# Kernel optimization log

Hardware: AMD Instinct MI355X
Metric: run time of the kernel (lower is better)

## Reference

```python
import jax, jax.numpy as jnp
import numpy as np

NUM_HEADS = 2

def mha(q, k, v, w_in, b_in, w_out, b_out):
    # torch nn.MultiheadAttention with batch_first=True, packed in_proj
    E = q.shape[-1]
    Dh = E // NUM_HEADS
    wq, wk, wv = jnp.split(w_in, 3, axis=0)
    bq, bk, bv = jnp.split(b_in, 3, axis=0)
    qh = (q @ wq.T + bq).reshape(q.shape[0], q.shape[1], NUM_HEADS, Dh)
    kh = (k @ wk.T + bk).reshape(k.shape[0], k.shape[1], NUM_HEADS, Dh)
    vh = (v @ wv.T + bv).reshape(v.shape[0], v.shape[1], NUM_HEADS, Dh)
    scores = jnp.einsum('blhd,bmhd->bhlm', qh, kh) / jnp.sqrt(jnp.asarray(Dh, q.dtype))
    attn = jax.nn.softmax(scores, axis=-1)
    ctx = jnp.einsum('bhlm,bmhd->blhd', attn, vh).reshape(q.shape[0], q.shape[1], E)
    return ctx @ w_out.T + b_out


def setup_inputs() -> dict:
    key = jax.random.key(0)
    ks = jax.random.split(key, 10)
    B, S, F, E, H = 16384, 512, 4, 8, 16
    s = 0.3
    return {
        'x': jax.random.normal(ks[0], (B, S, E), jnp.float32),
        'Q': jax.random.normal(ks[1], (F, E), jnp.float32) * s,
        'sa_w_in': jax.random.normal(ks[2], (3 * E, E), jnp.float32) * s,
        'sa_b_in': jnp.zeros((3 * E,), jnp.float32),
        'sa_w_out': jax.random.normal(ks[3], (E, E), jnp.float32) * s,
        'sa_b_out': jnp.zeros((E,), jnp.float32),
        'ca_w_in': jax.random.normal(ks[4], (3 * E, E), jnp.float32) * s,
        'ca_b_in': jnp.zeros((3 * E,), jnp.float32),
        'ca_w_out': jax.random.normal(ks[5], (E, E), jnp.float32) * s,
        'ca_b_out': jnp.zeros((E,), jnp.float32),
        'r_w1': jax.random.normal(ks[6], (H, F * E), jnp.float32) * s,
        'r_b1': jnp.zeros((H,), jnp.float32),
        'r_w2': jax.random.normal(ks[7], (1, H), jnp.float32) * s,
        'r_b2': jnp.zeros((1,), jnp.float32),
    }


def reference(x, Q, sa_w_in, sa_b_in, sa_w_out, sa_b_out,
              ca_w_in, ca_b_in, ca_w_out, ca_b_out,
              r_w1, r_b1, r_w2, r_b2):
    B = x.shape[0]
    # self-attention over the (batch-identical) factor queries
    Qb = jnp.broadcast_to(Q[None], (B,) + Q.shape)  # [B, F, E]
    Q_upd = mha(Qb, Qb, Qb, sa_w_in, sa_b_in, sa_w_out, sa_b_out)
    # cross-attention: factors attend over the input sequence
    Q_cross = mha(Q_upd, x, x, ca_w_in, ca_b_in, ca_w_out, ca_b_out)  # [B, F, E]
    similarity = jnp.einsum('bfe,bse->bfs', Q_cross, x)  # [B, F, S]
    attn_weights = jax.nn.softmax(similarity, axis=-1)
    final_factors = jnp.einsum('bfs,bse->bfe', attn_weights, x)  # [B, F, E]
    fused = final_factors.reshape(B, -1)  # [B, F*E]
    h = jax.nn.relu(fused @ r_w1.T + r_b1)
    out = h @ r_w2.T + r_b2  # [B, 1]
    return out, similarity
```

## Files before the change

kernel.cpp:

```cpp
#include <hip/hip_runtime.h>

#define SEQ 512
#define EMB 8
#define NFAC 4


__global__ void precompute_kernel(
    const float* __restrict__ Q,
    const float* __restrict__ sa_w_in, const float* __restrict__ sa_b_in,
    const float* __restrict__ sa_w_out, const float* __restrict__ sa_b_out,
    const float* __restrict__ ca_w_in, const float* __restrict__ ca_b_in,
    const float* __restrict__ ca_w_out, const float* __restrict__ ca_b_out,
    float* __restrict__ ws)
{
    const int t = threadIdx.x;
    __shared__ float sw[608];
    __shared__ float sqh[32], skh[32], svh[32], sctx[32], sQu[32], sqc[32];
    enum { OQ = 0, SWIN = 32, SBIN = 224, SWOUT = 248, SBOUT = 312,
           CWIN = 320, CBIN = 512, CWOUT = 536, CBOUT = 600 };

    for (int i = t; i < 32;  i += 64) sw[OQ + i]    = Q[i];
    for (int i = t; i < 192; i += 64) sw[SWIN + i]  = sa_w_in[i];
    for (int i = t; i < 24;  i += 64) sw[SBIN + i]  = sa_b_in[i];
    for (int i = t; i < 64;  i += 64) sw[SWOUT + i] = sa_w_out[i];
    if (t < 8) sw[SBOUT + t] = sa_b_out[t];
    for (int i = t; i < 192; i += 64) sw[CWIN + i]  = ca_w_in[i];
    for (int i = t; i < 24;  i += 64) sw[CBIN + i]  = ca_b_in[i];
    for (int i = t; i < 64;  i += 64) sw[CWOUT + i] = ca_w_out[i];
    if (t < 8) sw[CBOUT + t] = ca_b_out[t];
    __syncthreads();

    {
        const int e2 = t >> 3, e = t & 7;
        float m0 = 0.f, m1 = 0.f;
        #pragma unroll
        for (int d = 0; d < 4; ++d) {
            m0 += sw[CWOUT + e2 * 8 + d]     * sw[CWIN + (16 + d) * 8 + e];
            m1 += sw[CWOUT + e2 * 8 + 4 + d] * sw[CWIN + (20 + d) * 8 + e];
        }
        ws[72 + t]  = m0;
        ws[136 + t] = m1;
    }
    if (t < 8) {
        float a = sw[CBOUT + t];
        #pragma unroll
        for (int d = 0; d < 8; ++d) a += sw[CWOUT + t * 8 + d] * sw[CBIN + 16 + d];
        ws[200 + t] = a;
    }

    if (t < 32) {
        const int l = t >> 3, j = t & 7;
        float aq = sw[SBIN + j], ak = sw[SBIN + 8 + j], av = sw[SBIN + 16 + j];
        #pragma unroll
        for (int e = 0; e < 8; ++e) {
            const float q = sw[OQ + l * 8 + e];
            aq += q * sw[SWIN + j * 8 + e];
            ak += q * sw[SWIN + (8 + j) * 8 + e];
            av += q * sw[SWIN + (16 + j) * 8 + e];
        }
        sqh[t] = aq; skh[t] = ak; svh[t] = av;
    }
    __syncthreads();

    if (t < 8) {
        const int h = t >> 2, l = t & 3;
        float sc[4], mx = -1e30f;
        #pragma unroll
        for (int m = 0; m < 4; ++m) {
            float a = 0.f;
            #pragma unroll
            for (int d = 0; d < 4; ++d) a += sqh[l * 8 + h * 4 + d] * skh[m * 8 + h * 4 + d];
            sc[m] = 0.5f * a;
            mx = fmaxf(mx, sc[m]);
        }
        float ssum = 0.f;
        #pragma unroll
        for (int m = 0; m < 4; ++m) { sc[m] = __expf(sc[m] - mx); ssum += sc[m]; }
        const float inv = 1.f / ssum;
        #pragma unroll
        for (int d = 0; d < 4; ++d) {
            float a = 0.f;
            #pragma unroll
            for (int m = 0; m < 4; ++m) a += sc[m] * svh[m * 8 + h * 4 + d];
            sctx[l * 8 + h * 4 + d] = a * inv;
        }
    }
    __syncthreads();

    if (t < 32) {
        const int l = t >> 3, e2 = t & 7;
        float a = sw[SBOUT + e2];
        #pragma unroll
        for (int e = 0; e < 8; ++e) a += sctx[l * 8 + e] * sw[SWOUT + e2 * 8 + e];
        sQu[l * 8 + e2] = a;
    }
    __syncthreads();

    if (t < 32) {
        const int l = t >> 3, j = t & 7;
        float a = sw[CBIN + j];
        #pragma unroll
        for (int e = 0; e < 8; ++e) a += sQu[l * 8 + e] * sw[CWIN + j * 8 + e];
        sqc[l * 8 + j] = a;
    }
    __syncthreads();

    {
        const int p = t >> 3, e = t & 7, h = p >> 2, f = p & 3;
        float a = 0.f;
        #pragma unroll
        for (int d = 0; d < 4; ++d)
            a += sqc[f * 8 + h * 4 + d] * sw[CWIN + (8 + h * 4 + d) * 8 + e];
        ws[p * 8 + e] = 0.5f * a;
    }
    if (t < 8) {
        const int p = t, h = p >> 2, f = p & 3;
        float a = 0.f;
        #pragma unroll
        for (int d = 0; d < 4; ++d) a += sqc[f * 8 + h * 4 + d] * sw[CBIN + 8 + h * 4 + d];
        ws[64 + p] = 0.5f * a;
    }
}

__global__ __launch_bounds__(256, 4) void fused_kernel(
    const float* __restrict__ x,
    const float* __restrict__ r_w1, const float* __restrict__ r_b1,
    const float* __restrict__ r_w2, const float* __restrict__ r_b2,
    const float* __restrict__ ws,
    float* __restrict__ out, float* __restrict__ sim_out)
{
    const int b = blockIdx.x;
    const int tid = threadIdx.x;
    const int w = __builtin_amdgcn_readfirstlane(tid >> 6);
    const int lane = tid & 63;

    __shared__ float4 su4[16];
    __shared__ float sff[4][8];

    const float* xb = x + (size_t)b * (SEQ * EMB);

    const int p0 = 2 * w, p1 = 2 * w + 1;
    float wq0[8], wq1[8];
    #pragma unroll
    for (int e = 0; e < 8; ++e) { wq0[e] = ws[p0 * 8 + e]; wq1[e] = ws[p1 * 8 + e]; }
    const float cb0 = ws[64 + p0], cb1 = ws[64 + p1];

    float xr[8][8];
    float xa0[8] = {0.f,0.f,0.f,0.f,0.f,0.f,0.f,0.f};
    float xa1[8] = {0.f,0.f,0.f,0.f,0.f,0.f,0.f,0.f};
    float sum0 = 0.f, sum1 = 0.f;
    #pragma unroll
    for (int j = 0; j < 8; ++j) {
        const int s = lane + 64 * j;
        const float4* xp = (const float4*)(xb + s * 8);
        float4 lo = xp[0], hi = xp[1];
        xr[j][0] = lo.x; xr[j][1] = lo.y; xr[j][2] = lo.z; xr[j][3] = lo.w;
        xr[j][4] = hi.x; xr[j][5] = hi.y; xr[j][6] = hi.z; xr[j][7] = hi.w;
        float sc0 = cb0, sc1 = cb1;
        #pragma unroll
        for (int e = 0; e < 8; ++e) { sc0 += wq0[e] * xr[j][e]; sc1 += wq1[e] * xr[j][e]; }
        const float e0 = __expf(sc0), e1 = __expf(sc1);
        sum0 += e0; sum1 += e1;
        #pragma unroll
        for (int e = 0; e < 8; ++e) {
            xa0[e] += e0 * xr[j][e];
            xa1[e] += e1 * xr[j][e];
        }
    }
    #pragma unroll
    for (int m = 1; m < 64; m <<= 1) {
        sum0 += __shfl_xor(sum0, m, 64);
        sum1 += __shfl_xor(sum1, m, 64);
        #pragma unroll
        for (int e = 0; e < 8; ++e) {
            xa0[e] += __shfl_xor(xa0[e], m, 64);
            xa1[e] += __shfl_xor(xa1[e], m, 64);
        }
    }
    if (lane == 0) {
        const float i0 = 1.f / sum0, i1 = 1.f / sum1;
        su4[2 * p0]     = make_float4(xa0[0] * i0, xa0[1] * i0, xa0[2] * i0, xa0[3] * i0);
        su4[2 * p0 + 1] = make_float4(xa0[4] * i0, xa0[5] * i0, xa0[6] * i0, xa0[7] * i0);
        su4[2 * p1]     = make_float4(xa1[0] * i1, xa1[1] * i1, xa1[2] * i1, xa1[3] * i1);
        su4[2 * p1 + 1] = make_float4(xa1[4] * i1, xa1[5] * i1, xa1[6] * i1, xa1[7] * i1);
    }
    __syncthreads();

    const float* su = (const float*)su4;
    float u0[8], u1[8];
    #pragma unroll
    for (int e = 0; e < 8; ++e) { u0[e] = su[w * 8 + e]; u1[e] = su[(4 + w) * 8 + e]; }
    const int e2 = lane & 7;
    float qv = ws[200 + e2];
    #pragma unroll
    for (int e = 0; e < 8; ++e)
        qv += ws[72 + e2 * 8 + e] * u0[e] + ws[136 + e2 * 8 + e] * u1[e];
    float qcr[8];
    #pragma unroll
    for (int e = 0; e < 8; ++e) qcr[e] = __shfl(qv, e, 64);

    float facc[8] = {0.f,0.f,0.f,0.f,0.f,0.f,0.f,0.f};
    float fsum = 0.f;
    float* simb = sim_out + (size_t)b * (NFAC * SEQ) + w * SEQ;
    #pragma unroll
    for (int j = 0; j < 8; ++j) {
        const int s = lane + 64 * j;
        float sim = 0.f;
        #pragma unroll
        for (int e = 0; e < 8; ++e) sim += qcr[e] * xr[j][e];
        simb[s] = sim;
        const float ez = __expf(sim);
        fsum += ez;
        #pragma unroll
        for (int e = 0; e < 8; ++e) facc[e] += ez * xr[j][e];
    }
    #pragma unroll
    for (int m = 1; m < 64; m <<= 1) {
        fsum += __shfl_xor(fsum, m, 64);
        #pragma unroll
        for (int e = 0; e < 8; ++e) facc[e] += __shfl_xor(facc[e], m, 64);
    }
    if (lane == 0) {
        const float inv = 1.f / fsum;
        #pragma unroll
        for (int e = 0; e < 8; ++e) sff[w][e] = facc[e] * inv;
    }
    __syncthreads();

    if (tid < 16) {
        float a = r_b1[tid];
        const float* fusedp = &sff[0][0];
        const float4* w1p = (const float4*)(r_w1 + tid * 32);
        #pragma unroll
        for (int k = 0; k < 8; ++k) {
            float4 ww = w1p[k];
            a += ww.x * fusedp[4 * k + 0] + ww.y * fusedp[4 * k + 1]
               + ww.z * fusedp[4 * k + 2] + ww.w * fusedp[4 * k + 3];
        }
        a = fmaxf(a, 0.f);
        float v = a * r_w2[tid];
        v += __shfl_xor(v, 1, 64);
        v += __shfl_xor(v, 2, 64);
        v += __shfl_xor(v, 4, 64);
        v += __shfl_xor(v, 8, 64);
        if (tid == 0) out[b] = v + r_b2[0];
    }
}

extern "C" void kernel_launch(void* const* d_in, const int* in_sizes, int n_in,
                              void* d_out, int out_size, void* d_ws, size_t ws_size,
                              hipStream_t stream) {
    const float* x        = (const float*)d_in[0];
    const float* Q        = (const float*)d_in[1];
    const float* sa_w_in  = (const float*)d_in[2];
    const float* sa_b_in  = (const float*)d_in[3];
    const float* sa_w_out = (const float*)d_in[4];
    const float* sa_b_out = (const float*)d_in[5];
    const float* ca_w_in  = (const float*)d_in[6];
    const float* ca_b_in  = (const float*)d_in[7];
    const float* ca_w_out = (const float*)d_in[8];
    const float* ca_b_out = (const float*)d_in[9];
    const float* r_w1     = (const float*)d_in[10];
    const float* r_b1     = (const float*)d_in[11];
    const float* r_w2     = (const float*)d_in[12];
    const float* r_b2     = (const float*)d_in[13];

    float* out = (float*)d_out;
    const int B = in_sizes[0] / (SEQ * EMB);
    float* sim = out + B;
    float* ws  = (float*)d_ws;

    precompute_kernel<<<1, 64, 0, stream>>>(Q, sa_w_in, sa_b_in, sa_w_out, sa_b_out,
                                            ca_w_in, ca_b_in, ca_w_out, ca_b_out, ws);
    fused_kernel<<<B, 256, 0, stream>>>(x, r_w1, r_b1, r_w2, r_b2, ws, out, sim);
}
```

Before: 453.5 us.

## Reload x in second pass and shrink wave reductions to raise occupancy

Stops keeping the full 64-float x tile in registers across both passes and reloads it from global memory (likely an L2 hit) in the similarity pass. This frees registers, so the launch bound is raised from 4 to 8 blocks per SIMD. The butterfly reductions now run full shuffles only over the first 8 lanes, then select one component per lane so each later step shuffles one value instead of eight. Weights are made scalar via readfirstlane. The cost is a second pass of x reads.

```diff
diff --git a/kernel.cpp b/kernel.cpp
--- a/kernel.cpp
+++ b/kernel.cpp
@@ -4,6 +4,9 @@
 #define EMB 8
 #define NFAC 4
 
+__device__ __forceinline__ float rfl(float v) {
+    return __int_as_float(__builtin_amdgcn_readfirstlane(__float_as_int(v)));
+}
 
 __global__ void precompute_kernel(
     const float* __restrict__ Q,
@@ -122,7 +125,7 @@
     }
 }
 
-__global__ __launch_bounds__(256, 4) void fused_kernel(
+__global__ __launch_bounds__(256, 8) void fused_kernel(
     const float* __restrict__ x,
     const float* __restrict__ r_w1, const float* __restrict__ r_b1,
     const float* __restrict__ r_w2, const float* __restrict__ r_b2,
@@ -133,19 +136,22 @@
     const int tid = threadIdx.x;
     const int w = __builtin_amdgcn_readfirstlane(tid >> 6);
     const int lane = tid & 63;
-
-    __shared__ float4 su4[16];
-    __shared__ float sff[4][8];
+    const int c7 = lane & 7;
+
+    __shared__ float su[64];
+    __shared__ float sff[32];
 
     const float* xb = x + (size_t)b * (SEQ * EMB);
 
     const int p0 = 2 * w, p1 = 2 * w + 1;
     float wq0[8], wq1[8];
     #pragma unroll
-    for (int e = 0; e < 8; ++e) { wq0[e] = ws[p0 * 8 + e]; wq1[e] = ws[p1 * 8 + e]; }
-    const float cb0 = ws[64 + p0], cb1 = ws[64 + p1];
-
-    float xr[8][8];
+    for (int e = 0; e < 8; ++e) {
+        wq0[e] = rfl(ws[p0 * 8 + e]);
+        wq1[e] = rfl(ws[p1 * 8 + e]);
+    }
+    const float cb0 = rfl(ws[64 + p0]), cb1 = rfl(ws[64 + p1]);
+
     float xa0[8] = {0.f,0.f,0.f,0.f,0.f,0.f,0.f,0.f};
     float xa1[8] = {0.f,0.f,0.f,0.f,0.f,0.f,0.f,0.f};
     float sum0 = 0.f, sum1 = 0.f;
@@ -154,21 +160,20 @@
         const int s = lane + 64 * j;
         const float4* xp = (const float4*)(xb + s * 8);
         float4 lo = xp[0], hi = xp[1];
-        xr[j][0] = lo.x; xr[j][1] = lo.y; xr[j][2] = lo.z; xr[j][3] = lo.w;
-        xr[j][4] = hi.x; xr[j][5] = hi.y; xr[j][6] = hi.z; xr[j][7] = hi.w;
+        float xv[8] = {lo.x, lo.y, lo.z, lo.w, hi.x, hi.y, hi.z, hi.w};
         float sc0 = cb0, sc1 = cb1;
         #pragma unroll
-        for (int e = 0; e < 8; ++e) { sc0 += wq0[e] * xr[j][e]; sc1 += wq1[e] * xr[j][e]; }
+        for (int e = 0; e < 8; ++e) { sc0 += wq0[e] * xv[e]; sc1 += wq1[e] * xv[e]; }
         const float e0 = __expf(sc0), e1 = __expf(sc1);
         sum0 += e0; sum1 += e1;
         #pragma unroll
         for (int e = 0; e < 8; ++e) {
-            xa0[e] += e0 * xr[j][e];
-            xa1[e] += e1 * xr[j][e];
-        }
-    }
-    #pragma unroll
-    for (int m = 1; m < 64; m <<= 1) {
+            xa0[e] += e0 * xv[e];
+            xa1[e] += e1 * xv[e];
+        }
+    }
+    #pragma unroll
+    for (int m = 1; m < 8; m <<= 1) {
         sum0 += __shfl_xor(sum0, m, 64);
         sum1 += __shfl_xor(sum1, m, 64);
         #pragma unroll
@@ -177,24 +182,32 @@
             xa1[e] += __shfl_xor(xa1[e], m, 64);
         }
     }
-    if (lane == 0) {
-        const float i0 = 1.f / sum0, i1 = 1.f / sum1;
-        su4[2 * p0]     = make_float4(xa0[0] * i0, xa0[1] * i0, xa0[2] * i0, xa0[3] * i0);
-        su4[2 * p0 + 1] = make_float4(xa0[4] * i0, xa0[5] * i0, xa0[6] * i0, xa0[7] * i0);
-        su4[2 * p1]     = make_float4(xa1[0] * i1, xa1[1] * i1, xa1[2] * i1, xa1[3] * i1);
-        su4[2 * p1 + 1] = make_float4(xa1[4] * i1, xa1[5] * i1, xa1[6] * i1, xa1[7] * i1);
-    }
-    __syncthreads();
-
-    const float* su = (const float*)su4;
+    float v0 = xa0[0], v1 = xa1[0];
+    #pragma unroll
+    for (int e = 1; e < 8; ++e) {
+        v0 = (c7 == e) ? xa0[e] : v0;
+        v1 = (c7 == e) ? xa1[e] : v1;
+    }
+    #pragma unroll
+    for (int m = 8; m < 64; m <<= 1) {
+        sum0 += __shfl_xor(sum0, m, 64);
+        sum1 += __shfl_xor(sum1, m, 64);
+        v0 += __shfl_xor(v0, m, 64);
+        v1 += __shfl_xor(v1, m, 64);
+    }
+    if (lane < 8) {
+        su[p0 * 8 + lane] = v0 / sum0;
+        su[p1 * 8 + lane] = v1 / sum1;
+    }
+    __syncthreads();
+
     float u0[8], u1[8];
     #pragma unroll
-    for (int e = 0; e < 8; ++e) { u0[e] = su[w * 8 + e]; u1[e] = su[(4 + w) * 8 + e]; }
-    const int e2 = lane & 7;
-    float qv = ws[200 + e2];
+    for (int e = 0; e < 8; ++e) { u0[e] = su[w * 8 + e]; u1[e] = su[32 + w * 8 + e]; }
+    float qv = ws[200 + c7];
     #pragma unroll
     for (int e = 0; e < 8; ++e)
-        qv += ws[72 + e2 * 8 + e] * u0[e] + ws[136 + e2 * 8 + e] * u1[e];
+        qv += ws[72 + c7 * 8 + e] * u0[e] + ws[136 + c7 * 8 + e] * u1[e];
     float qcr[8];
     #pragma unroll
     for (int e = 0; e < 8; ++e) qcr[e] = __shfl(qv, e, 64);
@@ -205,37 +218,43 @@
     #pragma unroll
     for (int j = 0; j < 8; ++j) {
         const int s = lane + 64 * j;
+        const float4* xp = (const float4*)(xb + s * 8);
+        float4 lo = xp[0], hi = xp[1];
+        float xv[8] = {lo.x, lo.y, lo.z, lo.w, hi.x, hi.y, hi.z, hi.w};
         float sim = 0.f;
         #pragma unroll
-        for (int e = 0; e < 8; ++e) sim += qcr[e] * xr[j][e];
+        for (int e = 0; e < 8; ++e) sim += qcr[e] * xv[e];
         simb[s] = sim;
         const float ez = __expf(sim);
         fsum += ez;
         #pragma unroll
-        for (int e = 0; e < 8; ++e) facc[e] += ez * xr[j][e];
-    }
-    #pragma unroll
-    for (int m = 1; m < 64; m <<= 1) {
+        for (int e = 0; e < 8; ++e) facc[e] += ez * xv[e];
+    }
+    #pragma unroll
+    for (int m = 1; m < 8; m <<= 1) {
         fsum += __shfl_xor(fsum, m, 64);
         #pragma unroll
         for (int e = 0; e < 8; ++e) facc[e] += __shfl_xor(facc[e], m, 64);
     }
-    if (lane == 0) {
-        const float inv = 1.f / fsum;
-        #pragma unroll
-        for (int e = 0; e < 8; ++e) sff[w][e] = facc[e] * inv;
-    }
+    float fv = facc[0];
+    #pragma unroll
+    for (int e = 1; e < 8; ++e) fv = (c7 == e) ? facc[e] : fv;
+    #pragma unroll
+    for (int m = 8; m < 64; m <<= 1) {
+        fsum += __shfl_xor(fsum, m, 64);
+        fv += __shfl_xor(fv, m, 64);
+    }
+    if (lane < 8) sff[w * 8 + lane] = fv / fsum;
     __syncthreads();
 
     if (tid < 16) {
         float a = r_b1[tid];
-        const float* fusedp = &sff[0][0];
         const float4* w1p = (const float4*)(r_w1 + tid * 32);
         #pragma unroll
         for (int k = 0; k < 8; ++k) {
             float4 ww = w1p[k];
-            a += ww.x * fusedp[4 * k + 0] + ww.y * fusedp[4 * k + 1]
-               + ww.z * fusedp[4 * k + 2] + ww.w * fusedp[4 * k + 3];
+            a += ww.x * sff[4 * k + 0] + ww.y * sff[4 * k + 1]
+               + ww.z * sff[4 * k + 2] + ww.w * sff[4 * k + 3];
         }
         a = fmaxf(a, 0.f);
         float v = a * r_w2[tid];
```

Result: slower. 503.8 us (+11.1%).
